# Kernel optimization log

Measured on AMD Instinct MI355X. Metric: run time of the kernel, lower is better.

Reference implementation:

```python
import jax, jax.numpy as jnp
import numpy as np

HIDDEN = 32  # channel dim; rfft -> 17 complex bins

def setup_inputs() -> dict:
    key = jax.random.key(0)
    ks = jax.random.split(key, 5)
    x = jax.random.normal(ks[0], (64, 8192, HIDDEN), dtype=jnp.float32)
    half = HIDDEN // 2 + 1  # 17
    # parameters initialized like torch.randn * 0.02
    cm1_real = jax.random.normal(ks[1], (1, 1, half), dtype=jnp.float32) * 0.02
    cm1_imag = jax.random.normal(ks[2], (1, 1, half), dtype=jnp.float32) * 0.02
    cm2_real = jax.random.normal(ks[3], (1, 1, half), dtype=jnp.float32) * 0.02
    cm2_imag = jax.random.normal(ks[4], (1, 1, half), dtype=jnp.float32) * 0.02
    return {"x": x, "cm1_real": cm1_real, "cm1_imag": cm1_imag,
            "cm2_real": cm2_real, "cm2_imag": cm2_imag}

def reference(x, cm1_real, cm1_imag, cm2_real, cm2_imag):
    # complex mixing weights (nn.Parameter(torch.complex(real, imag)))
    cm1 = jax.lax.complex(cm1_real, cm1_imag)  # [1,1,17]
    cm2 = jax.lax.complex(cm2_real, cm2_imag)  # [1,1,17]
    # DFT_ along channel dim (orthonormal real FFT)
    xf = jnp.fft.rfft(x, axis=-1, norm="ortho")            # [B,F,17] complex64
    # Sine nonlinearity (w0=1) on complex values, sandwiched by complex gates
    xf = jnp.sin(xf * cm1) * cm2
    # IDFT_ back to length HIDDEN channels
    return jnp.fft.irfft(xf, n=HIDDEN, axis=-1, norm="ortho")  # [B,F,32] float32
```

## Files before the change

kernel.cpp:

```cpp
#include <hip/hip_runtime.h>
#include <math.h>

#define NCH 32
#define HALF 17
#define RPB 64
#define PAD 33

constexpr float CT[32] = {
   1.0f,                 0.9807852804032304f,  0.9238795325112867f,  0.8314696123025452f,
   0.7071067811865476f,  0.5555702330196022f,  0.3826834323650898f,  0.1950903220161283f,
   0.0f,                -0.1950903220161283f, -0.3826834323650898f, -0.5555702330196022f,
  -0.7071067811865476f, -0.8314696123025452f, -0.9238795325112867f, -0.9807852804032304f,
  -1.0f,                -0.9807852804032304f, -0.9238795325112867f, -0.8314696123025452f,
  -0.7071067811865476f, -0.5555702330196022f, -0.3826834323650898f, -0.1950903220161283f,
   0.0f,                 0.1950903220161283f,  0.3826834323650898f,  0.5555702330196022f,
   0.7071067811865476f,  0.8314696123025452f,  0.9238795325112867f,  0.9807852804032304f
};
constexpr float ST[32] = {
   0.0f,                 0.1950903220161283f,  0.3826834323650898f,  0.5555702330196022f,
   0.7071067811865476f,  0.8314696123025452f,  0.9238795325112867f,  0.9807852804032304f,
   1.0f,                 0.9807852804032304f,  0.9238795325112867f,  0.8314696123025452f,
   0.7071067811865476f,  0.5555702330196022f,  0.3826834323650898f,  0.1950903220161283f,
   0.0f,                -0.1950903220161283f, -0.3826834323650898f, -0.5555702330196022f,
  -0.7071067811865476f, -0.8314696123025452f, -0.9238795325112867f, -0.9807852804032304f,
  -1.0f,                -0.9807852804032304f, -0.9238795325112867f, -0.8314696123025452f,
  -0.7071067811865476f, -0.5555702330196022f, -0.3826834323650898f, -0.1950903220161283f
};

__device__ __forceinline__ void cnonlin(float sr, float si,
    float w1r, float w1i, float w2r, float w2i, float& G, float& H)
{
    const float p = fmaf(sr, w1r, si * w1i);
    const float q = fmaf(sr, w1i, -(si * w1r));
    float sp, cp;
    __sincosf(p, &sp, &cp);
    const float eq = __expf(q), en = __expf(-q);
    const float sA = sp * (eq + en);
    const float sB = cp * (eq - en);
    G = fmaf(sA, w2r, -(sB * w2i));
    H = fmaf(sA, w2i, sB * w2r);
}

__device__ __forceinline__ float cnonlin_real(float sr,
    float w1r, float w1i, float w2r, float w2i)
{
    const float p = sr * w1r;
    const float q = sr * w1i;
    float sp, cp;
    __sincosf(p, &sp, &cp);
    const float eq = __expf(q), en = __expf(-q);
    return fmaf(sp * (eq + en), w2r, -((cp * (eq - en)) * w2i));
}

__global__ __launch_bounds__(RPB, 3) void fcm_kernel(
    const float* __restrict__ x,
    const float* __restrict__ c1r, const float* __restrict__ c1i,
    const float* __restrict__ c2r, const float* __restrict__ c2i,
    float* __restrict__ out)
{
    __shared__ float tile[RPB * PAD];
    const int t = threadIdx.x;
    const long long base = (long long)blockIdx.x * (RPB * NCH);
    const float inv = 0.17677669529663687f;

    #pragma unroll
    for (int i = 0; i < 8; ++i) {
        const int ft = (i * RPB + t) * 4;
        float4 v = *reinterpret_cast<const float4*>(x + base + ft);
        const int row = ft >> 5, col = ft & 31;
        float* p = &tile[row * PAD + col];
        p[0] = v.x; p[1] = v.y; p[2] = v.z; p[3] = v.w;
    }
    __syncthreads();

    float xr[NCH];
    #pragma unroll
    for (int j = 0; j < NCH; ++j) xr[j] = tile[t * PAD + j];

    float ev[16], od[16];
    #pragma unroll
    for (int m = 1; m <= 15; ++m) {
        ev[m] = xr[m] + xr[32 - m];
        od[m] = xr[m] - xr[32 - m];
    }
    const float xp = xr[0] + xr[16], xm = xr[0] - xr[16];
    const float e8 = ev[8], o8 = od[8];
    float ep[8], em[8], opp[8], om[8];
    #pragma unroll
    for (int m = 1; m <= 7; ++m) {
        ep[m]  = ev[m] + ev[16 - m];
        em[m]  = ev[m] - ev[16 - m];
        opp[m] = od[m] + od[16 - m];
        om[m]  = od[m] - od[16 - m];
    }

    float Gp[8], Gm[8], Hp[8], Hm[8];
    float G0, G16, G8, H8;

    {
        const float A  = ep[2] + ep[4] + ep[6];
        const float B  = ep[1] + ep[3] + ep[5] + ep[7];
        const float b0 = xp + e8;
        const float sr0  = b0 + A + B;
        const float sr16 = b0 + A - B;
        G0  = cnonlin_real(sr0,  c1r[0]  * inv, c1i[0]  * inv,
                           c2r[0]  * (0.5f * inv), c2i[0]  * (0.5f * inv));
        G16 = cnonlin_real(sr16, c1r[16] * inv, c1i[16] * inv,
                           c2r[16] * (0.5f * inv), c2i[16] * (0.5f * inv));
        const float sr8 = b0 - ep[2] + ep[4] - ep[6];
        const float si8 = om[1] - om[3] + om[5] - om[7];
        cnonlin(sr8, si8, c1r[8] * inv, c1i[8] * inv,
                c2r[8] * inv, c2i[8] * inv, G8, H8);
    }

    #pragma unroll
    for (int k = 1; k <= 7; ++k) {
        const int kp = 16 - k;
        const bool kodd = (k & 1);
        const float u1 = kodd ? em[1] : ep[1],  u3 = kodd ? em[3] : ep[3];
        const float u5 = kodd ? em[5] : ep[5],  u7 = kodd ? em[7] : ep[7];
        const float u2 = kodd ? em[2] : ep[2],  u4 = kodd ? em[4] : ep[4];
        const float u6 = kodd ? em[6] : ep[6];
        const float v1 = kodd ? opp[1] : om[1], v3 = kodd ? opp[3] : om[3];
        const float v5 = kodd ? opp[5] : om[5], v7 = kodd ? opp[7] : om[7];
        const float v2 = kodd ? opp[2] : om[2], v4 = kodd ? opp[4] : om[4];
        const float v6 = kodd ? opp[6] : om[6];

        const float SrE = fmaf(CT[(2*k)&31], u2, fmaf(CT[(4*k)&31], u4, CT[(6*k)&31] * u6));
        const float SrO = fmaf(CT[k&31], u1, fmaf(CT[(3*k)&31], u3,
                          fmaf(CT[(5*k)&31], u5, CT[(7*k)&31] * u7)));
        const float SiE = fmaf(ST[(2*k)&31], v2, fmaf(ST[(4*k)&31], v4, ST[(6*k)&31] * v6));
        const float SiO = fmaf(ST[k&31], v1, fmaf(ST[(3*k)&31], v3,
                          fmaf(ST[(5*k)&31], v5, ST[(7*k)&31] * v7)));

        const float tb = kodd ? xm : (xp + (((k & 2) == 0) ? e8 : -e8));
        float SiEO  = SiE + SiO;
        float SiOmE = SiO - SiE;
        if (kodd) {
            const float s8 = ((k & 2) == 0) ? o8 : -o8;
            SiEO  += s8;
            SiOmE -= s8;
        }
        const float srk  = tb + SrE + SrO;
        const float srkp = tb + (SrE - SrO);

        float Gk, Hk, Gkp, Hkp;
        cnonlin(srk,  SiEO,  c1r[k]  * inv, c1i[k]  * inv,
                c2r[k]  * inv, c2i[k]  * inv, Gk,  Hk);
        cnonlin(srkp, SiOmE, c1r[kp] * inv, c1i[kp] * inv,
                c2r[kp] * inv, c2i[kp] * inv, Gkp, Hkp);
        Gp[k] = Gk + Gkp;  Gm[k] = Gk - Gkp;
        Hp[k] = Hk + Hkp;  Hm[k] = Hk - Hkp;
    }

    float* row = &tile[t * PAD];
    const float Dp = G0 + G16, Dm = G0 - G16;

    {
        const float GA = Gp[2] + Gp[4] + Gp[6];
        const float GB = Gp[1] + Gp[3] + Gp[5] + Gp[7];
        const float b8 = Dp + G8;
        row[0]  = b8 + GA + GB;
        row[16] = b8 + GA - GB;
        const float C8 = -Gp[2] + Gp[4] - Gp[6];
        const float S8 =  Hm[1] - Hm[3] + Hm[5] - Hm[7];
        const float t8 = b8 + C8;
        row[8]  = t8 - S8;
        row[24] = t8 + S8;
    }

    #pragma unroll
    for (int n = 1; n <= 7; ++n) {
        const bool nodd = (n & 1);
        const float g1 = nodd ? Gm[1] : Gp[1], g3 = nodd ? Gm[3] : Gp[3];
        const float g5 = nodd ? Gm[5] : Gp[5], g7 = nodd ? Gm[7] : Gp[7];
        const float g2 = nodd ? Gm[2] : Gp[2], g4 = nodd ? Gm[4] : Gp[4];
        const float g6 = nodd ? Gm[6] : Gp[6];
        const float h1 = nodd ? Hp[1] : Hm[1], h3 = nodd ? Hp[3] : Hm[3];
        const float h5 = nodd ? Hp[5] : Hm[5], h7 = nodd ? Hp[7] : Hm[7];
        const float h2 = nodd ? Hp[2] : Hm[2], h4 = nodd ? Hp[4] : Hm[4];
        const float h6 = nodd ? Hp[6] : Hm[6];

        const float CE = fmaf(CT[(2*n)&31], g2, fmaf(CT[(4*n)&31], g4, CT[(6*n)&31] * g6));
        const float CO = fmaf(CT[n&31], g1, fmaf(CT[(3*n)&31], g3,
                         fmaf(CT[(5*n)&31], g5, CT[(7*n)&31] * g7)));
        const float SE = fmaf(ST[(2*n)&31], h2, fmaf(ST[(4*n)&31], h4, ST[(6*n)&31] * h6));
        const float SO = fmaf(ST[n&31], h1, fmaf(ST[(3*n)&31], h3,
                         fmaf(ST[(5*n)&31], h5, ST[(7*n)&31] * h7)));

        const float a = CE + CO, b = CE - CO, c = SE + SO, d = SE - SO;
        float w1, w2;
        if (nodd) {
            const float P = ((n & 2) == 0) ? H8 : -H8;
            w1 = Dm - P;  w2 = Dm + P;
        } else {
            w1 = Dp + (((n & 2) == 0) ? G8 : -G8);
            w2 = w1;
        }
        row[n]      = w1 + a - c;
        row[32 - n] = w2 + a + c;
        row[16 - n] = w2 + b + d;
        row[16 + n] = w1 + b - d;
    }
    __syncthreads();

    #pragma unroll
    for (int i = 0; i < 8; ++i) {
        const int ft = (i * RPB + t) * 4;
        const int r = ft >> 5, col = ft & 31;
        const float* p = &tile[r * PAD + col];
        float4 v;
        v.x = p[0]; v.y = p[1]; v.z = p[2]; v.w = p[3];
        *reinterpret_cast<float4*>(out + base + ft) = v;
    }
}

extern "C" void kernel_launch(void* const* d_in, const int* in_sizes, int n_in,
                              void* d_out, int out_size, void* d_ws, size_t ws_size,
                              hipStream_t stream) {
    const float* x   = (const float*)d_in[0];
    const float* c1r = (const float*)d_in[1];
    const float* c1i = (const float*)d_in[2];
    const float* c2r = (const float*)d_in[3];
    const float* c2i = (const float*)d_in[4];
    float* out = (float*)d_out;

    const int total  = in_sizes[0];
    const int blocks = total / (RPB * NCH);
    fcm_kernel<<<blocks, RPB, 0, stream>>>(x, c1r, c1i, c2r, c2i, out);
}
```

Baseline: 118.3 us.

## Drop LDS transpose tile and load each row directly with float4 per thread

Removes the shared-memory staging tile and both block barriers; each thread now reads its own 32-float row straight from global memory with eight float4 loads and writes its output the same way. The block size grows from 64 to 256 threads with a new launch bound. This removes LDS traffic and synchronisation, but global accesses become strided by 128 bytes across lanes, so each wavefront load instruction touches many cache lines instead of fully coalesced contiguous ones, relying on L1/L2 to absorb the inefficiency.

```diff
diff --git a/kernel.cpp b/kernel.cpp
--- a/kernel.cpp
+++ b/kernel.cpp
@@ -2,9 +2,7 @@
 #include <math.h>
 
 #define NCH 32
-#define HALF 17
-#define RPB 64
-#define PAD 33
+#define TPB 256
 
 constexpr float CT[32] = {
    1.0f,                 0.9807852804032304f,  0.9238795325112867f,  0.8314696123025452f,
@@ -52,30 +50,24 @@
     return fmaf(sp * (eq + en), w2r, -((cp * (eq - en)) * w2i));
 }
 
-__global__ __launch_bounds__(RPB, 3) void fcm_kernel(
+__global__ __launch_bounds__(TPB, 4) void fcm_kernel(
     const float* __restrict__ x,
     const float* __restrict__ c1r, const float* __restrict__ c1i,
     const float* __restrict__ c2r, const float* __restrict__ c2i,
     float* __restrict__ out)
 {
-    __shared__ float tile[RPB * PAD];
-    const int t = threadIdx.x;
-    const long long base = (long long)blockIdx.x * (RPB * NCH);
+    const long long row = (long long)blockIdx.x * TPB + threadIdx.x;
+    const float* xp_ptr = x + row * NCH;
+    float*       op_ptr = out + row * NCH;
     const float inv = 0.17677669529663687f;
 
+    float xr[NCH];
     #pragma unroll
     for (int i = 0; i < 8; ++i) {
-        const int ft = (i * RPB + t) * 4;
-        float4 v = *reinterpret_cast<const float4*>(x + base + ft);
-        const int row = ft >> 5, col = ft & 31;
-        float* p = &tile[row * PAD + col];
-        p[0] = v.x; p[1] = v.y; p[2] = v.z; p[3] = v.w;
-    }
-    __syncthreads();
-
-    float xr[NCH];
-    #pragma unroll
-    for (int j = 0; j < NCH; ++j) xr[j] = tile[t * PAD + j];
+        float4 v = *reinterpret_cast<const float4*>(xp_ptr + i * 4);
+        xr[i * 4 + 0] = v.x; xr[i * 4 + 1] = v.y;
+        xr[i * 4 + 2] = v.z; xr[i * 4 + 3] = v.w;
+    }
 
     float ev[16], od[16];
     #pragma unroll
@@ -153,20 +145,20 @@
         Hp[k] = Hk + Hkp;  Hm[k] = Hk - Hkp;
     }
 
-    float* row = &tile[t * PAD];
+    float y[NCH];
     const float Dp = G0 + G16, Dm = G0 - G16;
 
     {
         const float GA = Gp[2] + Gp[4] + Gp[6];
         const float GB = Gp[1] + Gp[3] + Gp[5] + Gp[7];
         const float b8 = Dp + G8;
-        row[0]  = b8 + GA + GB;
-        row[16] = b8 + GA - GB;
+        y[0]  = b8 + GA + GB;
+        y[16] = b8 + GA - GB;
         const float C8 = -Gp[2] + Gp[4] - Gp[6];
         const float S8 =  Hm[1] - Hm[3] + Hm[5] - Hm[7];
         const float t8 = b8 + C8;
-        row[8]  = t8 - S8;
-        row[24] = t8 + S8;
+        y[8]  = t8 - S8;
+        y[24] = t8 + S8;
     }
 
     #pragma unroll
@@ -197,21 +189,18 @@
             w1 = Dp + (((n & 2) == 0) ? G8 : -G8);
             w2 = w1;
         }
-        row[n]      = w1 + a - c;
-        row[32 - n] = w2 + a + c;
-        row[16 - n] = w2 + b + d;
-        row[16 + n] = w1 + b - d;
-    }
-    __syncthreads();
+        y[n]      = w1 + a - c;
+        y[32 - n] = w2 + a + c;
+        y[16 - n] = w2 + b + d;
+        y[16 + n] = w1 + b - d;
+    }
 
     #pragma unroll
     for (int i = 0; i < 8; ++i) {
-        const int ft = (i * RPB + t) * 4;
-        const int r = ft >> 5, col = ft & 31;
-        const float* p = &tile[r * PAD + col];
         float4 v;
-        v.x = p[0]; v.y = p[1]; v.z = p[2]; v.w = p[3];
-        *reinterpret_cast<float4*>(out + base + ft) = v;
+        v.x = y[i * 4 + 0]; v.y = y[i * 4 + 1];
+        v.z = y[i * 4 + 2]; v.w = y[i * 4 + 3];
+        *reinterpret_cast<float4*>(op_ptr + i * 4) = v;
     }
 }
 
@@ -226,6 +215,6 @@
     float* out = (float*)d_out;
 
     const int total  = in_sizes[0];
-    const int blocks = total / (RPB * NCH);
-    fcm_kernel<<<blocks, RPB, 0, stream>>>(x, c1r, c1i, c2r, c2i, out);
-}
+    const int blocks = total / (TPB * NCH);
+    fcm_kernel<<<blocks, TPB, 0, stream>>>(x, c1r, c1i, c2r, c2i, out);
+}
```

New measurement: 130.3 us. +10.2%, slower.
